# Performance work log

Hardware: AMD Instinct MI355X
Metric: run time of the kernel (lower is better)

The kernel has to match this reference:

```python
import jax, jax.numpy as jnp
import numpy as np

NQ, NKV, D = 32, 8, 64
HID = 2048
EPS = 1e-5
THETA = 1000000.0


def _rmsnorm(x, w):
    var = jnp.mean(x * x, axis=-1, keepdims=True)
    return x * jax.lax.rsqrt(var + EPS) * w


def setup_inputs() -> dict:
    key = jax.random.key(0)
    k1, k2, k3 = jax.random.split(key, 3)
    T = 2048
    positions = jnp.arange(T, dtype=jnp.int64) if jax.config.jax_enable_x64 else jnp.arange(T, dtype=jnp.int32)
    hidden_states = jax.random.normal(k1, (T, HID), dtype=jnp.float32)
    w_qkv = jax.random.normal(k2, (HID, (NQ + 2 * NKV) * D), dtype=jnp.float32) / np.sqrt(HID)
    w_out = jax.random.normal(k3, (NQ * D, HID), dtype=jnp.float32) / np.sqrt(NQ * D)
    q_ln_w = jnp.ones((D,), dtype=jnp.float32)
    k_ln_w = jnp.ones((D,), dtype=jnp.float32)
    return {"positions": positions, "hidden_states": hidden_states, "w_qkv": w_qkv,
            "w_out": w_out, "q_ln_w": q_ln_w, "k_ln_w": k_ln_w}


def reference(positions, hidden_states, w_qkv, w_out, q_ln_w, k_ln_w):
    T = hidden_states.shape[0]
    qkv = hidden_states @ w_qkv  # [T, (NQ+2*NKV)*D]
    q = qkv[:, : NQ * D].reshape(T, NQ, D)
    k = qkv[:, NQ * D : (NQ + NKV) * D].reshape(T, NKV, D)
    v = qkv[:, (NQ + NKV) * D :].reshape(T, NKV, D)
    # per-head RMSNorm on q and k
    q = _rmsnorm(q, q_ln_w)
    k = _rmsnorm(k, k_ln_w)
    # neox-style RoPE (rotate halves)
    inv_freq = 1.0 / (THETA ** (jnp.arange(0, D, 2, dtype=jnp.float32) / D))
    ang = positions.astype(jnp.float32)[:, None] * inv_freq  # [T, D/2]
    cos = jnp.cos(ang)[:, None, :]
    sin = jnp.sin(ang)[:, None, :]
    def rope(x):
        x1, x2 = x[..., : D // 2], x[..., D // 2 :]
        return jnp.concatenate([x1 * cos - x2 * sin, x2 * cos + x1 * sin], axis=-1)
    q = rope(q)
    k = rope(k)
    # grouped-query causal attention (one sequence, positions define order)
    G = NQ // NKV
    qg = q.reshape(T, NKV, G, D)
    scores = jnp.einsum('tkgd,skd->kgts', qg, k) * (D ** -0.5)  # [NKV,G,T,T]
    causal = jnp.arange(T)[:, None] >= jnp.arange(T)[None, :]
    scores = jnp.where(causal[None, None], scores, -1e30)
    probs = jax.nn.softmax(scores, axis=-1)
    attn = jnp.einsum('kgts,skd->tkgd', probs, v).reshape(T, NQ * D)
    return attn @ w_out
```

## Files before the change

### kernel.cpp

```cpp
#include <hip/hip_runtime.h>

typedef __bf16 bhalf;
typedef __bf16 bhalf8 __attribute__((ext_vector_type(8)));
typedef __bf16 bhalf4 __attribute__((ext_vector_type(4)));
typedef float f32x4 __attribute__((ext_vector_type(4)));

typedef __attribute__((address_space(1))) const void* gas_p;
typedef __attribute__((address_space(3))) void* las_p;

#define T_SEQ 2048
#define HIDN  2048
#define NQH   32
#define NKVH  8
#define DH    64
#define NQKV  3072

__global__ __launch_bounds__(256) void cast_bf16_k(const float* __restrict__ in,
                                                   bhalf* __restrict__ out, int n) {
  int i = (blockIdx.x * 256 + threadIdx.x) * 4;
  if (i + 3 < n) {
    float4 v = *(const float4*)(in + i);
    bhalf4 o;
    o[0] = (bhalf)v.x; o[1] = (bhalf)v.y; o[2] = (bhalf)v.z; o[3] = (bhalf)v.w;
    *(bhalf4*)(out + i) = o;
  }
}

__global__ __launch_bounds__(256) void transpose_cast_k(const float* __restrict__ in,
                                                        bhalf* __restrict__ out, int R, int C) {
  __shared__ float tile[32][33];
  int bx = blockIdx.x * 32;
  int by = blockIdx.y * 32;
  int tx = threadIdx.x & 31, ty = threadIdx.x >> 5;
#pragma unroll
  for (int p = 0; p < 4; ++p)
    tile[ty + 8 * p][tx] = in[(size_t)(by + ty + 8 * p) * C + bx + tx];
  __syncthreads();
#pragma unroll
  for (int p = 0; p < 4; ++p)
    out[(size_t)(bx + ty + 8 * p) * R + by + tx] = (bhalf)tile[tx][ty + 8 * p];
}

__device__ __forceinline__ void gemm_core(const bhalf* __restrict__ A,
                                          const bhalf* __restrict__ Bt, int K,
                                          int bm, int bn, int tid,
                                          bhalf* As, bhalf* Bs, f32x4 acc[2][4]) {
  int lane = tid & 63, wv = tid >> 6;
  int m16 = lane & 15, q4 = lane >> 4;
  int srow = tid >> 3;
  int scol = ((tid & 7) ^ (srow & 7)) * 8;
  const bhalf* asrc = A + (size_t)(bm + srow) * K + scol;
  const bhalf* bsrc = Bt + (size_t)(bn + srow) * K + scol;
  bhalf* adst = As + (wv * 8) * 64;
  bhalf* bdst = Bs + (wv * 8) * 64;
  int swz = m16 & 7;

  auto stage = [&](int k0, int sbuf) {
#pragma unroll
    for (int c = 0; c < 4; ++c)
      __builtin_amdgcn_global_load_lds((gas_p)(asrc + (size_t)(c * 32) * K + k0),
                                       (las_p)(adst + sbuf * 8192 + c * 2048), 16, 0, 0);
#pragma unroll
    for (int c = 0; c < 2; ++c)
      __builtin_amdgcn_global_load_lds((gas_p)(bsrc + (size_t)(c * 32) * K + k0),
                                       (las_p)(bdst + sbuf * 4096 + c * 2048), 16, 0, 0);
  };

  stage(0, 0);
  int buf = 0;
  for (int k0 = 0; k0 < K; k0 += 64) {
    __syncthreads();
    if (k0 + 64 < K) stage(k0 + 64, buf ^ 1);
    const bhalf* Ab = As + buf * 8192;
    const bhalf* Bb = Bs + buf * 4096;
    bhalf8 af[2][2], bf[4][2];
#pragma unroll
    for (int mi = 0; mi < 2; ++mi)
#pragma unroll
      for (int ks = 0; ks < 2; ++ks)
        af[mi][ks] = *(const bhalf8*)&Ab[(wv * 32 + mi * 16 + m16) * 64 +
                                         (((ks * 4 + q4) ^ swz) * 8)];
#pragma unroll
    for (int ni = 0; ni < 4; ++ni)
#pragma unroll
      for (int ks = 0; ks < 2; ++ks)
        bf[ni][ks] = *(const bhalf8*)&Bb[(ni * 16 + m16) * 64 +
                                         (((ks * 4 + q4) ^ swz) * 8)];
#pragma unroll
    for (int mi = 0; mi < 2; ++mi)
#pragma unroll
      for (int ni = 0; ni < 4; ++ni) {
        acc[mi][ni] = __builtin_amdgcn_mfma_f32_16x16x32_bf16(af[mi][0], bf[ni][0], acc[mi][ni], 0, 0, 0);
        acc[mi][ni] = __builtin_amdgcn_mfma_f32_16x16x32_bf16(af[mi][1], bf[ni][1], acc[mi][ni], 0, 0, 0);
      }
    buf ^= 1;
  }
}

__global__ __launch_bounds__(256) void gemm1_fused_k(const bhalf* __restrict__ A,
                                                     const bhalf* __restrict__ Bt,
                                                     const int* __restrict__ pos,
                                                     const float* __restrict__ qw,
                                                     const float* __restrict__ kw,
                                                     bhalf* __restrict__ qo,
                                                     bhalf* __restrict__ ko,
                                                     bhalf* __restrict__ vt) {
  __shared__ __align__(16) bhalf As[2 * 128 * 64];
  __shared__ __align__(16) bhalf Bs[2 * 64 * 64];
  int tid = threadIdx.x, lane = tid & 63, wv = tid >> 6;
  int m16 = lane & 15, q4 = lane >> 4;
  int bm = blockIdx.y * 128, bn = blockIdx.x * 64, h = blockIdx.x;
  f32x4 zero4 = {0.f, 0.f, 0.f, 0.f};
  f32x4 acc[2][4];
#pragma unroll
  for (int mi = 0; mi < 2; ++mi)
#pragma unroll
    for (int ni = 0; ni < 4; ++ni) acc[mi][ni] = zero4;

  gemm_core(A, Bt, HIDN, bm, bn, tid, As, Bs, acc);

  int wr0 = wv * 32;
  if (h < 40) {
    float wd[4];
    const float* wptr = (h < 32) ? qw : kw;
    float wscale = (h < 32) ? 0.18033688011112042f : 1.0f;
#pragma unroll
    for (int ni = 0; ni < 4; ++ni) wd[ni] = wptr[ni * 16 + m16] * wscale;
    float f0 = exp2f((float)m16 * -0.6228615177913804f);
    float f1 = f0 * 0.001f;
#pragma unroll
    for (int mi = 0; mi < 2; ++mi)
#pragma unroll
      for (int r = 0; r < 4; ++r) {
        int trow = bm + wr0 + mi * 16 + q4 * 4 + r;
        float x0 = acc[mi][0][r], x1 = acc[mi][1][r], x2 = acc[mi][2][r], x3 = acc[mi][3][r];
        float ss = x0 * x0 + x1 * x1 + x2 * x2 + x3 * x3;
        ss += __shfl_xor(ss, 1);
        ss += __shfl_xor(ss, 2);
        ss += __shfl_xor(ss, 4);
        ss += __shfl_xor(ss, 8);
        float sc = rsqrtf(ss * (1.0f / 64.0f) + 1e-5f);
        float y0 = x0 * sc * wd[0], y1 = x1 * sc * wd[1];
        float y2 = x2 * sc * wd[2], y3 = x3 * sc * wd[3];
        float p = (float)pos[trow];
        float a0 = p * f0, a1 = p * f1;
        float c0 = cosf(a0), s0 = sinf(a0), c1 = cosf(a1), s1 = sinf(a1);
        float o0 = y0 * c0 - y2 * s0, o2 = y2 * c0 + y0 * s0;
        float o1 = y1 * c1 - y3 * s1, o3 = y3 * c1 + y1 * s1;
        bhalf* dst = (h < 32) ? (qo + (size_t)trow * 2048 + h * 64 + m16)
                              : (ko + (size_t)trow * 512 + (h - 32) * 64 + m16);
        dst[0] = (bhalf)o0; dst[16] = (bhalf)o1; dst[32] = (bhalf)o2; dst[48] = (bhalf)o3;
      }
  } else {
#pragma unroll
    for (int mi = 0; mi < 2; ++mi)
#pragma unroll
      for (int ni = 0; ni < 4; ++ni) {
        int trow0 = bm + wr0 + mi * 16 + q4 * 4;
        int d = (h - 40) * 64 + ni * 16 + m16;
        bhalf4 pk;
        pk[0] = (bhalf)acc[mi][ni][0]; pk[1] = (bhalf)acc[mi][ni][1];
        pk[2] = (bhalf)acc[mi][ni][2]; pk[3] = (bhalf)acc[mi][ni][3];
        *(bhalf4*)(vt + (size_t)d * 2048 + trow0) = pk;
      }
  }
}

__global__ __launch_bounds__(256) void gemm2_k(const bhalf* __restrict__ A,
                                               const bhalf* __restrict__ Bt,
                                               float* __restrict__ C) {
  __shared__ __align__(16) bhalf As[2 * 128 * 64];
  __shared__ __align__(16) bhalf Bs[2 * 64 * 64];
  int tid = threadIdx.x, lane = tid & 63, wv = tid >> 6;
  int m16 = lane & 15, q4 = lane >> 4;
  int bm = blockIdx.y * 128, bn = blockIdx.x * 64;
  f32x4 zero4 = {0.f, 0.f, 0.f, 0.f};
  f32x4 acc[2][4];
#pragma unroll
  for (int mi = 0; mi < 2; ++mi)
#pragma unroll
    for (int ni = 0; ni < 4; ++ni) acc[mi][ni] = zero4;

  gemm_core(A, Bt, HIDN, bm, bn, tid, As, Bs, acc);

  int wr0 = wv * 32;
#pragma unroll
  for (int mi = 0; mi < 2; ++mi)
#pragma unroll
    for (int r = 0; r < 4; ++r) {
      size_t base = (size_t)(bm + wr0 + mi * 16 + q4 * 4 + r) * 2048 + bn + m16;
      C[base] = acc[mi][0][r]; C[base + 16] = acc[mi][1][r];
      C[base + 32] = acc[mi][2][r]; C[base + 48] = acc[mi][3][r];
    }
}

__global__ __launch_bounds__(256) void attn_k(const bhalf* __restrict__ q,
                                              const bhalf* __restrict__ k,
                                              const bhalf* __restrict__ vt,
                                              bhalf* __restrict__ o) {
  __shared__ __align__(16) bhalf Kb[2][4096];
  __shared__ __align__(16) bhalf Vb[2][4096];
  __shared__ __align__(16) bhalf Pb[4][16][64];
  int tid = threadIdx.x, lane = tid & 63, w = tid >> 6;
  int h = blockIdx.x, kh = h >> 2;
  int qt = 31 - blockIdx.y;
  int qb = qt * 64;
  int m16 = lane & 15, q4 = lane >> 4;
  int wrow0 = qb + w * 16;

  const bhalf* qp = q + (size_t)(wrow0 + m16) * 2048 + h * 64;
  bhalf8 qf0 = *(const bhalf8*)(qp + q4 * 8);
  bhalf8 qf1 = *(const bhalf8*)(qp + 32 + q4 * 8);

  int srow = tid >> 3;
  int scol = ((tid & 7) ^ (srow & 7)) * 8;
  const bhalf* ksrc = k + (size_t)srow * 512 + kh * 64 + scol;
  const bhalf* vsrc = vt + (size_t)(kh * 64 + srow) * 2048 + scol;
  bhalf* kdst = &Kb[0][0] + w * 512;
  bhalf* vdst = &Vb[0][0] + w * 512;

  auto stage = [&](int c) {
    int buf = c & 1, s0 = c * 64;
#pragma unroll
    for (int j = 0; j < 2; ++j) {
      __builtin_amdgcn_global_load_lds((gas_p)(ksrc + (size_t)(s0 + j * 32) * 512),
                                       (las_p)(kdst + buf * 4096 + j * 2048), 16, 0, 0);
      __builtin_amdgcn_global_load_lds((gas_p)(vsrc + (size_t)(j * 32) * 2048 + s0),
                                       (las_p)(vdst + buf * 4096 + j * 2048), 16, 0, 0);
    }
  };

  f32x4 zero4 = {0.f, 0.f, 0.f, 0.f};
  f32x4 oac[4];
  float psum = 0.f;
#pragma unroll
  for (int ni = 0; ni < 4; ++ni) oac[ni] = zero4;
  int swz = m16 & 7;
  bhalf* prow = &Pb[w][m16][0];
  int woff = (q4 & 1) << 2;

  stage(0);
  for (int c = 0; c <= qt; ++c) {
    __syncthreads();
    if (c < qt) stage(c + 1);
    int buf = c & 1;
    if (c < qt) {
      bhalf8 kf[4][2];
#pragma unroll
      for (int st = 0; st < 4; ++st)
#pragma unroll
        for (int ks = 0; ks < 2; ++ks)
          kf[st][ks] = *(const bhalf8*)&Kb[buf][(st * 16 + m16) * 64 + (((ks * 4 + q4) ^ swz) * 8)];
      f32x4 sv[4];
      __builtin_amdgcn_s_setprio(1);
#pragma unroll
      for (int st = 0; st < 4; ++st) {
        f32x4 t0 = __builtin_amdgcn_mfma_f32_16x16x32_bf16(kf[st][0], qf0, zero4, 0, 0, 0);
        sv[st] = __builtin_amdgcn_mfma_f32_16x16x32_bf16(kf[st][1], qf1, t0, 0, 0, 0);
      }
      __builtin_amdgcn_s_setprio(0);
#pragma unroll
      for (int st = 0; st < 4; ++st) {
        bhalf4 pk;
#pragma unroll
        for (int r = 0; r < 4; ++r) {
          float pe = exp2f(sv[st][r]);
          psum += pe;
          pk[r] = (bhalf)pe;
        }
        *(bhalf4*)(prow + ((((2 * st + (q4 >> 1)) ^ swz) << 3) + woff)) = pk;
      }
      bhalf8 vf[4][2];
#pragma unroll
      for (int ni = 0; ni < 4; ++ni)
#pragma unroll
        for (int ks = 0; ks < 2; ++ks)
          vf[ni][ks] = *(const bhalf8*)&Vb[buf][(ni * 16 + m16) * 64 + (((ks * 4 + q4) ^ swz) * 8)];
      bhalf8 ap0 = *(const bhalf8*)(prow + ((q4 ^ swz) << 3));
      bhalf8 ap1 = *(const bhalf8*)(prow + (((4 + q4) ^ swz) << 3));
      __builtin_amdgcn_s_setprio(1);
#pragma unroll
      for (int ni = 0; ni < 4; ++ni) {
        oac[ni] = __builtin_amdgcn_mfma_f32_16x16x32_bf16(ap0, vf[ni][0], oac[ni], 0, 0, 0);
        oac[ni] = __builtin_amdgcn_mfma_f32_16x16x32_bf16(ap1, vf[ni][1], oac[ni], 0, 0, 0);
      }
      __builtin_amdgcn_s_setprio(0);
    } else {
      bhalf8 kf[4][2];
      f32x4 sv[4];
#pragma unroll
      for (int st = 0; st < 4; ++st)
        if (st <= w) {
#pragma unroll
          for (int ks = 0; ks < 2; ++ks)
            kf[st][ks] = *(const bhalf8*)&Kb[buf][(st * 16 + m16) * 64 + (((ks * 4 + q4) ^ swz) * 8)];
          f32x4 t0 = __builtin_amdgcn_mfma_f32_16x16x32_bf16(kf[st][0], qf0, zero4, 0, 0, 0);
          sv[st] = __builtin_amdgcn_mfma_f32_16x16x32_bf16(kf[st][1], qf1, t0, 0, 0, 0);
        }
      int stwr = (w >= 2) ? 3 : 1;
#pragma unroll
      for (int st = 0; st < 4; ++st) {
        if (st > stwr) continue;
        bhalf4 pk;
#pragma unroll
        for (int r = 0; r < 4; ++r) {
          float pe = 0.f;
          if (st < w) {
            pe = exp2f(sv[st][r]);
          } else if (st == w) {
            pe = (q4 * 4 + r <= m16) ? exp2f(sv[st][r]) : 0.f;
          }
          psum += pe;
          pk[r] = (bhalf)pe;
        }
        *(bhalf4*)(prow + ((((2 * st + (q4 >> 1)) ^ swz) << 3) + woff)) = pk;
      }
      int ksmax = (w >= 2) ? 1 : 0;
      bhalf8 vf[4][2];
#pragma unroll
      for (int ni = 0; ni < 4; ++ni)
#pragma unroll
        for (int ks = 0; ks < 2; ++ks)
          if (ks <= ksmax)
            vf[ni][ks] = *(const bhalf8*)&Vb[buf][(ni * 16 + m16) * 64 + (((ks * 4 + q4) ^ swz) * 8)];
      bhalf8 ap0 = *(const bhalf8*)(prow + ((q4 ^ swz) << 3));
#pragma unroll
      for (int ni = 0; ni < 4; ++ni)
        oac[ni] = __builtin_amdgcn_mfma_f32_16x16x32_bf16(ap0, vf[ni][0], oac[ni], 0, 0, 0);
      if (ksmax) {
        bhalf8 ap1 = *(const bhalf8*)(prow + (((4 + q4) ^ swz) << 3));
#pragma unroll
        for (int ni = 0; ni < 4; ++ni)
          oac[ni] = __builtin_amdgcn_mfma_f32_16x16x32_bf16(ap1, vf[ni][1], oac[ni], 0, 0, 0);
      }
    }
  }
  psum += __shfl_xor(psum, 16);
  psum += __shfl_xor(psum, 32);
  float inv = 1.0f / psum;
  float invr[4];
#pragma unroll
  for (int r = 0; r < 4; ++r) invr[r] = __shfl(inv, q4 * 4 + r);
#pragma unroll
  for (int ni = 0; ni < 4; ++ni)
#pragma unroll
    for (int r = 0; r < 4; ++r) {
      int trow = wrow0 + q4 * 4 + r;
      o[(size_t)trow * 2048 + h * 64 + ni * 16 + m16] = (bhalf)(oac[ni][r] * invr[r]);
    }
}

extern "C" void kernel_launch(void* const* d_in, const int* in_sizes, int n_in,
                              void* d_out, int out_size, void* d_ws, size_t ws_size,
                              hipStream_t stream) {
  const int* positions = (const int*)d_in[0];
  const float* hidden  = (const float*)d_in[1];
  const float* w_qkv   = (const float*)d_in[2];
  const float* w_out   = (const float*)d_in[3];
  const float* q_ln    = (const float*)d_in[4];
  const float* k_ln    = (const float*)d_in[5];
  float* out = (float*)d_out;

  char* wsp = (char*)d_ws;
  bhalf* hid_bf  = (bhalf*)(wsp);
  bhalf* wqkvT   = (bhalf*)(wsp + 8388608);
  bhalf* woutT   = (bhalf*)(wsp + 20971520);
  bhalf* q_bf    = (bhalf*)(wsp + 29360128);
  bhalf* k_bf    = (bhalf*)(wsp + 37748736);
  bhalf* vt_g    = (bhalf*)(wsp + 41943040);
  bhalf* attn_bf = (bhalf*)(wsp + 44040192);

  cast_bf16_k<<<T_SEQ * HIDN / 1024, 256, 0, stream>>>(hidden, hid_bf, T_SEQ * HIDN);
  transpose_cast_k<<<dim3(NQKV / 32, HIDN / 32), 256, 0, stream>>>(w_qkv, wqkvT, HIDN, NQKV);
  transpose_cast_k<<<dim3(HIDN / 32, HIDN / 32), 256, 0, stream>>>(w_out, woutT, HIDN, HIDN);
  gemm1_fused_k<<<dim3(NQKV / 64, T_SEQ / 128), 256, 0, stream>>>(
      hid_bf, wqkvT, positions, q_ln, k_ln, q_bf, k_bf, vt_g);
  attn_k<<<dim3(NQH, 32), 256, 0, stream>>>(q_bf, k_bf, vt_g, attn_bf);
  gemm2_k<<<dim3(HIDN / 64, T_SEQ / 128), 256, 0, stream>>>(attn_bf, woutT, out);
}
```

Measured before the change: 217.4 us.

## Enlarge GEMM tiles to 128x128 with XCD-aware block remap and fuse prep kernels

Both GEMMs move from 128x64 to 128x128 output tiles, with each wave computing a 64x64 sub-tile (4x4 MFMA accumulators). This raises operand reuse from LDS and halves the number of blocks. Block IDs are remapped across the 8 XCDs so neighbouring tiles share L2. The three cast/transpose prep kernels are merged into one launch to cut launch overhead. The larger accumulator set raises register pressure and the LDS footprint doubles for B, which may lower occupancy; with fewer blocks the CUs may also be less evenly loaded.

```diff
diff --git a/kernel.cpp b/kernel.cpp
--- a/kernel.cpp
+++ b/kernel.cpp
@@ -15,22 +15,34 @@
 #define DH    64
 #define NQKV  3072
 
-__global__ __launch_bounds__(256) void cast_bf16_k(const float* __restrict__ in,
-                                                   bhalf* __restrict__ out, int n) {
-  int i = (blockIdx.x * 256 + threadIdx.x) * 4;
-  if (i + 3 < n) {
-    float4 v = *(const float4*)(in + i);
+__global__ __launch_bounds__(256) void prep_k(const float* __restrict__ hidden,
+                                              const float* __restrict__ w_qkv,
+                                              const float* __restrict__ w_out,
+                                              bhalf* __restrict__ hid_bf,
+                                              bhalf* __restrict__ wqkvT,
+                                              bhalf* __restrict__ woutT) {
+  __shared__ float tile[32][33];
+  int bid = blockIdx.x;
+  if (bid < 4096) {
+    int i = (bid * 256 + threadIdx.x) * 4;
+    float4 v = *(const float4*)(hidden + i);
     bhalf4 o;
     o[0] = (bhalf)v.x; o[1] = (bhalf)v.y; o[2] = (bhalf)v.z; o[3] = (bhalf)v.w;
-    *(bhalf4*)(out + i) = o;
-  }
-}
-
-__global__ __launch_bounds__(256) void transpose_cast_k(const float* __restrict__ in,
-                                                        bhalf* __restrict__ out, int R, int C) {
-  __shared__ float tile[32][33];
-  int bx = blockIdx.x * 32;
-  int by = blockIdx.y * 32;
+    *(bhalf4*)(hid_bf + i) = o;
+    return;
+  }
+  const float* in;
+  bhalf* out;
+  int R, C, bx, by;
+  if (bid < 10240) {
+    int b2 = bid - 4096;
+    in = w_qkv; out = wqkvT; R = HIDN; C = NQKV;
+    bx = (b2 % 96) * 32; by = (b2 / 96) * 32;
+  } else {
+    int b2 = bid - 10240;
+    in = w_out; out = woutT; R = HIDN; C = HIDN;
+    bx = (b2 % 64) * 32; by = (b2 / 64) * 32;
+  }
   int tx = threadIdx.x & 31, ty = threadIdx.x >> 5;
 #pragma unroll
   for (int p = 0; p < 4; ++p)
@@ -44,9 +56,10 @@
 __device__ __forceinline__ void gemm_core(const bhalf* __restrict__ A,
                                           const bhalf* __restrict__ Bt, int K,
                                           int bm, int bn, int tid,
-                                          bhalf* As, bhalf* Bs, f32x4 acc[2][4]) {
+                                          bhalf* As, bhalf* Bs, f32x4 acc[4][4]) {
   int lane = tid & 63, wv = tid >> 6;
   int m16 = lane & 15, q4 = lane >> 4;
+  int wm = (wv >> 1) * 64, wn = (wv & 1) * 64;
   int srow = tid >> 3;
   int scol = ((tid & 7) ^ (srow & 7)) * 8;
   const bhalf* asrc = A + (size_t)(bm + srow) * K + scol;
@@ -61,9 +74,9 @@
       __builtin_amdgcn_global_load_lds((gas_p)(asrc + (size_t)(c * 32) * K + k0),
                                        (las_p)(adst + sbuf * 8192 + c * 2048), 16, 0, 0);
 #pragma unroll
-    for (int c = 0; c < 2; ++c)
+    for (int c = 0; c < 4; ++c)
       __builtin_amdgcn_global_load_lds((gas_p)(bsrc + (size_t)(c * 32) * K + k0),
-                                       (las_p)(bdst + sbuf * 4096 + c * 2048), 16, 0, 0);
+                                       (las_p)(bdst + sbuf * 8192 + c * 2048), 16, 0, 0);
   };
 
   stage(0, 0);
@@ -72,27 +85,22 @@
     __syncthreads();
     if (k0 + 64 < K) stage(k0 + 64, buf ^ 1);
     const bhalf* Ab = As + buf * 8192;
-    const bhalf* Bb = Bs + buf * 4096;
-    bhalf8 af[2][2], bf[4][2];
-#pragma unroll
-    for (int mi = 0; mi < 2; ++mi)
-#pragma unroll
-      for (int ks = 0; ks < 2; ++ks)
-        af[mi][ks] = *(const bhalf8*)&Ab[(wv * 32 + mi * 16 + m16) * 64 +
-                                         (((ks * 4 + q4) ^ swz) * 8)];
-#pragma unroll
-    for (int ni = 0; ni < 4; ++ni)
-#pragma unroll
-      for (int ks = 0; ks < 2; ++ks)
-        bf[ni][ks] = *(const bhalf8*)&Bb[(ni * 16 + m16) * 64 +
-                                         (((ks * 4 + q4) ^ swz) * 8)];
-#pragma unroll
-    for (int mi = 0; mi < 2; ++mi)
-#pragma unroll
-      for (int ni = 0; ni < 4; ++ni) {
-        acc[mi][ni] = __builtin_amdgcn_mfma_f32_16x16x32_bf16(af[mi][0], bf[ni][0], acc[mi][ni], 0, 0, 0);
-        acc[mi][ni] = __builtin_amdgcn_mfma_f32_16x16x32_bf16(af[mi][1], bf[ni][1], acc[mi][ni], 0, 0, 0);
-      }
+    const bhalf* Bb = Bs + buf * 8192;
+#pragma unroll
+    for (int ks = 0; ks < 2; ++ks) {
+      bhalf8 af[4], bf[4];
+#pragma unroll
+      for (int mi = 0; mi < 4; ++mi)
+        af[mi] = *(const bhalf8*)&Ab[(wm + mi * 16 + m16) * 64 + (((ks * 4 + q4) ^ swz) * 8)];
+#pragma unroll
+      for (int ni = 0; ni < 4; ++ni)
+        bf[ni] = *(const bhalf8*)&Bb[(wn + ni * 16 + m16) * 64 + (((ks * 4 + q4) ^ swz) * 8)];
+#pragma unroll
+      for (int mi = 0; mi < 4; ++mi)
+#pragma unroll
+        for (int ni = 0; ni < 4; ++ni)
+          acc[mi][ni] = __builtin_amdgcn_mfma_f32_16x16x32_bf16(af[mi], bf[ni], acc[mi][ni], 0, 0, 0);
+    }
     buf ^= 1;
   }
 }
@@ -105,34 +113,38 @@
                                                      bhalf* __restrict__ qo,
                                                      bhalf* __restrict__ ko,
                                                      bhalf* __restrict__ vt) {
-  __shared__ __align__(16) bhalf As[2 * 128 * 64];
-  __shared__ __align__(16) bhalf Bs[2 * 64 * 64];
+  __shared__ __align__(16) bhalf As[2 * 8192];
+  __shared__ __align__(16) bhalf Bs[2 * 8192];
   int tid = threadIdx.x, lane = tid & 63, wv = tid >> 6;
   int m16 = lane & 15, q4 = lane >> 4;
-  int bm = blockIdx.y * 128, bn = blockIdx.x * 64, h = blockIdx.x;
+  int orig = blockIdx.x;
+  int wgid = (orig & 7) * 48 + (orig >> 3);
+  int bx = wgid % 24, by = wgid / 24;
+  int bm = by * 128, bn = bx * 128;
   f32x4 zero4 = {0.f, 0.f, 0.f, 0.f};
-  f32x4 acc[2][4];
-#pragma unroll
-  for (int mi = 0; mi < 2; ++mi)
+  f32x4 acc[4][4];
+#pragma unroll
+  for (int mi = 0; mi < 4; ++mi)
 #pragma unroll
     for (int ni = 0; ni < 4; ++ni) acc[mi][ni] = zero4;
 
   gemm_core(A, Bt, HIDN, bm, bn, tid, As, Bs, acc);
 
-  int wr0 = wv * 32;
-  if (h < 40) {
+  int r0 = bm + (wv >> 1) * 64;
+  int hh = (bn >> 6) + (wv & 1);
+  if (hh < 40) {
     float wd[4];
-    const float* wptr = (h < 32) ? qw : kw;
-    float wscale = (h < 32) ? 0.18033688011112042f : 1.0f;
+    const float* wptr = (hh < 32) ? qw : kw;
+    float wscale = (hh < 32) ? 0.18033688011112042f : 1.0f;
 #pragma unroll
     for (int ni = 0; ni < 4; ++ni) wd[ni] = wptr[ni * 16 + m16] * wscale;
     float f0 = exp2f((float)m16 * -0.6228615177913804f);
     float f1 = f0 * 0.001f;
 #pragma unroll
-    for (int mi = 0; mi < 2; ++mi)
+    for (int mi = 0; mi < 4; ++mi)
 #pragma unroll
       for (int r = 0; r < 4; ++r) {
-        int trow = bm + wr0 + mi * 16 + q4 * 4 + r;
+        int trow = r0 + mi * 16 + q4 * 4 + r;
         float x0 = acc[mi][0][r], x1 = acc[mi][1][r], x2 = acc[mi][2][r], x3 = acc[mi][3][r];
         float ss = x0 * x0 + x1 * x1 + x2 * x2 + x3 * x3;
         ss += __shfl_xor(ss, 1);
@@ -147,17 +159,17 @@
         float c0 = cosf(a0), s0 = sinf(a0), c1 = cosf(a1), s1 = sinf(a1);
         float o0 = y0 * c0 - y2 * s0, o2 = y2 * c0 + y0 * s0;
         float o1 = y1 * c1 - y3 * s1, o3 = y3 * c1 + y1 * s1;
-        bhalf* dst = (h < 32) ? (qo + (size_t)trow * 2048 + h * 64 + m16)
-                              : (ko + (size_t)trow * 512 + (h - 32) * 64 + m16);
+        bhalf* dst = (hh < 32) ? (qo + (size_t)trow * 2048 + hh * 64 + m16)
+                               : (ko + (size_t)trow * 512 + (hh - 32) * 64 + m16);
         dst[0] = (bhalf)o0; dst[16] = (bhalf)o1; dst[32] = (bhalf)o2; dst[48] = (bhalf)o3;
       }
   } else {
 #pragma unroll
-    for (int mi = 0; mi < 2; ++mi)
+    for (int mi = 0; mi < 4; ++mi)
 #pragma unroll
       for (int ni = 0; ni < 4; ++ni) {
-        int trow0 = bm + wr0 + mi * 16 + q4 * 4;
-        int d = (h - 40) * 64 + ni * 16 + m16;
+        int trow0 = r0 + mi * 16 + q4 * 4;
+        int d = (hh - 40) * 64 + ni * 16 + m16;
         bhalf4 pk;
         pk[0] = (bhalf)acc[mi][ni][0]; pk[1] = (bhalf)acc[mi][ni][1];
         pk[2] = (bhalf)acc[mi][ni][2]; pk[3] = (bhalf)acc[mi][ni][3];
@@ -169,26 +181,30 @@
 __global__ __launch_bounds__(256) void gemm2_k(const bhalf* __restrict__ A,
                                                const bhalf* __restrict__ Bt,
                                                float* __restrict__ C) {
-  __shared__ __align__(16) bhalf As[2 * 128 * 64];
-  __shared__ __align__(16) bhalf Bs[2 * 64 * 64];
+  __shared__ __align__(16) bhalf As[2 * 8192];
+  __shared__ __align__(16) bhalf Bs[2 * 8192];
   int tid = threadIdx.x, lane = tid & 63, wv = tid >> 6;
   int m16 = lane & 15, q4 = lane >> 4;
-  int bm = blockIdx.y * 128, bn = blockIdx.x * 64;
+  int orig = blockIdx.x;
+  int wgid = (orig & 7) * 32 + (orig >> 3);
+  int bx = wgid & 15, by = wgid >> 4;
+  int bm = by * 128, bn = bx * 128;
   f32x4 zero4 = {0.f, 0.f, 0.f, 0.f};
-  f32x4 acc[2][4];
-#pragma unroll
-  for (int mi = 0; mi < 2; ++mi)
+  f32x4 acc[4][4];
+#pragma unroll
+  for (int mi = 0; mi < 4; ++mi)
 #pragma unroll
     for (int ni = 0; ni < 4; ++ni) acc[mi][ni] = zero4;
 
   gemm_core(A, Bt, HIDN, bm, bn, tid, As, Bs, acc);
 
-  int wr0 = wv * 32;
-#pragma unroll
-  for (int mi = 0; mi < 2; ++mi)
+  int r0 = bm + (wv >> 1) * 64;
+  int c0 = bn + (wv & 1) * 64;
+#pragma unroll
+  for (int mi = 0; mi < 4; ++mi)
 #pragma unroll
     for (int r = 0; r < 4; ++r) {
-      size_t base = (size_t)(bm + wr0 + mi * 16 + q4 * 4 + r) * 2048 + bn + m16;
+      size_t base = (size_t)(r0 + mi * 16 + q4 * 4 + r) * 2048 + c0 + m16;
       C[base] = acc[mi][0][r]; C[base + 16] = acc[mi][1][r];
       C[base + 32] = acc[mi][2][r]; C[base + 48] = acc[mi][3][r];
     }
@@ -370,11 +386,9 @@
   bhalf* vt_g    = (bhalf*)(wsp + 41943040);
   bhalf* attn_bf = (bhalf*)(wsp + 44040192);
 
-  cast_bf16_k<<<T_SEQ * HIDN / 1024, 256, 0, stream>>>(hidden, hid_bf, T_SEQ * HIDN);
-  transpose_cast_k<<<dim3(NQKV / 32, HIDN / 32), 256, 0, stream>>>(w_qkv, wqkvT, HIDN, NQKV);
-  transpose_cast_k<<<dim3(HIDN / 32, HIDN / 32), 256, 0, stream>>>(w_out, woutT, HIDN, HIDN);
-  gemm1_fused_k<<<dim3(NQKV / 64, T_SEQ / 128), 256, 0, stream>>>(
+  prep_k<<<14336, 256, 0, stream>>>(hidden, w_qkv, w_out, hid_bf, wqkvT, woutT);
+  gemm1_fused_k<<<384, 256, 0, stream>>>(
       hid_bf, wqkvT, positions, q_ln, k_ln, q_bf, k_bf, vt_g);
   attn_k<<<dim3(NQH, 32), 256, 0, stream>>>(q_bf, k_bf, vt_g, attn_bf);
-  gemm2_k<<<dim3(HIDN / 64, T_SEQ / 128), 256, 0, stream>>>(attn_bf, woutT, out);
-}
+  gemm2_k<<<256, 256, 0, stream>>>(attn_bf, woutT, out);
+}
```

After: 353.9 us. +62.8%, slower.
